# Performance work log

Measured on AMD Instinct MI355X. Metric: run time of the kernel, lower is better.

The kernel has to match this reference:

```python
import jax, jax.numpy as jnp
import numpy as np

N_EMBD = 1024
N_HEAD = 16
HEAD_DIM = N_EMBD // N_HEAD


def setup_inputs() -> dict:
    key = jax.random.key(0)
    kx, kq, kk, kv, ko = jax.random.split(key, 5)
    B, S = 2, 2048
    return {
        "x": jax.random.normal(kx, (B, S, N_EMBD), dtype=jnp.float32),
        "W_q": jax.random.normal(kq, (N_EMBD, N_EMBD), dtype=jnp.float32),
        "W_k": jax.random.normal(kk, (N_EMBD, N_EMBD), dtype=jnp.float32),
        "W_v": jax.random.normal(kv, (N_EMBD, N_EMBD), dtype=jnp.float32),
        "W_o": jax.random.normal(ko, (N_EMBD, N_EMBD), dtype=jnp.float32),
    }


def reference(x, W_q, W_k, W_v, W_o):
    B, S, E = x.shape
    H, D = N_HEAD, HEAD_DIM
    scale = 1.0 / np.sqrt(D).astype(np.float32)
    # QKV projections, split into heads: (B, H, S, D)
    q = (x @ W_q).reshape(B, S, H, D).transpose(0, 2, 1, 3)
    k = (x @ W_k).reshape(B, S, H, D).transpose(0, 2, 1, 3)
    v = (x @ W_v).reshape(B, S, H, D).transpose(0, 2, 1, 3)
    # scaled scores with causal mask
    scores = jnp.einsum("bhqd,bhkd->bhqk", q, k) * scale
    causal = jnp.tril(jnp.ones((S, S), dtype=bool))
    scores = jnp.where(causal, scores, -jnp.inf)
    attn = jax.nn.softmax(scores, axis=-1)
    out = jnp.einsum("bhqk,bhkd->bhqd", attn, v)
    out = out.transpose(0, 2, 1, 3).reshape(B, S, E)
    return out @ W_o
```

## Files before the change

kernel.cpp:

```cpp
#include <hip/hip_runtime.h>
#include <stdint.h>

#define E 1024
#define S 2048
#define NH 16
#define HD 64

typedef _Float16 f16;
typedef _Float16 f16x4 __attribute__((ext_vector_type(4)));
typedef _Float16 f16x8 __attribute__((ext_vector_type(8)));
typedef __fp16 hv4 __attribute__((ext_vector_type(4)));
typedef float f32x4 __attribute__((ext_vector_type(4)));

__device__ __forceinline__ void async16(const void* g, void* l) {
  __builtin_amdgcn_global_load_lds(
      (const __attribute__((address_space(1))) unsigned int*)g,
      (__attribute__((address_space(3))) unsigned int*)l, 16, 0, 0);
}

__global__ __launch_bounds__(256) void cvt_all(
    const float* __restrict__ x, const float* __restrict__ Wq,
    const float* __restrict__ Wk, const float* __restrict__ Wv,
    const float* __restrict__ Wo, f16* __restrict__ xh, f16* __restrict__ xl,
    f16* __restrict__ Wh, f16* __restrict__ Wl) {
  const int z = blockIdx.z;
  const int tid = threadIdx.x;
  if (z == 4) {
    int base = ((blockIdx.y * 32 + blockIdx.x) * 256 + tid) * 16;
#pragma unroll
    for (int u = 0; u < 4; u++) {
      int i = base + u * 4;
      float4 a = *(const float4*)(x + i);
      f16 h0 = (f16)a.x, h1 = (f16)a.y, h2 = (f16)a.z, h3 = (f16)a.w;
      f16x4 hv = {h0, h1, h2, h3};
      f16x4 lv = {(f16)(a.x - (float)h0), (f16)(a.y - (float)h1),
                  (f16)(a.z - (float)h2), (f16)(a.w - (float)h3)};
      *(f16x4*)(xh + i) = hv;
      *(f16x4*)(xl + i) = lv;
    }
    return;
  }
  __shared__ float tile[32][33];
  const float* W = z == 0 ? Wq : z == 1 ? Wk : z == 2 ? Wv : Wo;
  const int tx = tid & 31, ty = tid >> 5;
  const int x0 = blockIdx.x * 32, y0 = blockIdx.y * 32;
#pragma unroll
  for (int i = 0; i < 4; i++)
    tile[ty + i * 8][tx] = W[(size_t)(y0 + ty + i * 8) * E + x0 + tx];
  __syncthreads();
  f16* outh = Wh + (size_t)z * E * E;
  f16* outl = Wl + (size_t)z * E * E;
#pragma unroll
  for (int i = 0; i < 4; i++) {
    float v = tile[tx][ty + i * 8];
    size_t o = (size_t)(x0 + ty + i * 8) * E + (y0 + tx);
    f16 hi = (f16)v;
    outh[o] = hi;
    if (z < 2) outl[o] = (f16)(v - (float)hi);
  }
}


template <bool SPLIT2>
__device__ __forceinline__ void gemm_mainloop(
    const f16* __restrict__ Ah, const f16* __restrict__ Al,
    const f16* __restrict__ Bh, const f16* __restrict__ Bl, int m0, int n0,
    int K, f16* Ahs, f16* Als, f16* Bhs, f16* Bls, f32x4 acc[4][4]) {
  const int tid = threadIdx.x, lane = tid & 63, wid = tid >> 6;
  const int quad = lane >> 4, c16 = lane & 15;
  const int rA = tid >> 2;
  const int cA = (tid & 3) ^ ((rA >> 1) & 3);
  const size_t gA0 = (size_t)(m0 + rA) * K + cA * 8;
  const size_t gA1 = (size_t)(m0 + 64 + rA) * K + cA * 8;
  const size_t gB0 = (size_t)(n0 + rA) * K + cA * 8;
  const size_t gB1 = (size_t)(n0 + 64 + rA) * K + cA * 8;
  const int l0 = tid * 8, l1 = (256 + tid) * 8;
  int a_off[4], b_off[4];
#pragma unroll
  for (int i = 0; i < 4; i++) {
    int ra = (wid >> 1) * 64 + i * 16 + c16;
    a_off[i] = ra * 32 + ((quad ^ ((ra >> 1) & 3)) << 3);
    int rb = (wid & 1) * 64 + i * 16 + c16;
    b_off[i] = rb * 32 + ((quad ^ ((rb >> 1) & 3)) << 3);
  }
  for (int k0 = 0; k0 < K; k0 += 32) {
    __syncthreads();
    async16(Ah + gA0 + k0, Ahs + l0);
    async16(Ah + gA1 + k0, Ahs + l1);
    async16(Bh + gB0 + k0, Bhs + l0);
    async16(Bh + gB1 + k0, Bhs + l1);
    if constexpr (SPLIT2) {
      async16(Al + gA0 + k0, Als + l0);
      async16(Al + gA1 + k0, Als + l1);
      async16(Bl + gB0 + k0, Bls + l0);
      async16(Bl + gB1 + k0, Bls + l1);
    }
    __syncthreads();
    f16x8 ah[4], bh[4];
#pragma unroll
    for (int i = 0; i < 4; i++) {
      ah[i] = *(const f16x8*)(Ahs + a_off[i]);
      bh[i] = *(const f16x8*)(Bhs + b_off[i]);
    }
    if constexpr (SPLIT2) {
      f16x8 al[4], bl[4];
#pragma unroll
      for (int i = 0; i < 4; i++) {
        al[i] = *(const f16x8*)(Als + a_off[i]);
        bl[i] = *(const f16x8*)(Bls + b_off[i]);
      }
#pragma unroll
      for (int i = 0; i < 4; i++)
#pragma unroll
        for (int j = 0; j < 4; j++) {
          acc[i][j] = __builtin_amdgcn_mfma_f32_16x16x32_f16(ah[i], bh[j], acc[i][j], 0, 0, 0);
          acc[i][j] = __builtin_amdgcn_mfma_f32_16x16x32_f16(ah[i], bl[j], acc[i][j], 0, 0, 0);
          acc[i][j] = __builtin_amdgcn_mfma_f32_16x16x32_f16(al[i], bh[j], acc[i][j], 0, 0, 0);
        }
    } else {
#pragma unroll
      for (int i = 0; i < 4; i++)
#pragma unroll
        for (int j = 0; j < 4; j++)
          acc[i][j] = __builtin_amdgcn_mfma_f32_16x16x32_f16(ah[i], bh[j], acc[i][j], 0, 0, 0);
    }
  }
}

__global__ __launch_bounds__(256) void qkv_gemm(
    const f16* __restrict__ xh, const f16* __restrict__ xl,
    const f16* __restrict__ Wh, const f16* __restrict__ Wl,
    f16* __restrict__ Qh, f16* __restrict__ Ql, f16* __restrict__ Kh,
    f16* __restrict__ Kl, f16* __restrict__ Vt) {
  __shared__ __align__(16) char smem_raw[36864];
  f16* Ahs = (f16*)smem_raw;
  f16* Als = Ahs + 4096;
  f16* Bhs = Ahs + 8192;
  f16* Bls = Ahs + 12288;
  const int z = blockIdx.z;
  const int m0 = blockIdx.y * 128, n0 = blockIdx.x * 128;
  const f16* Bth = Wh + (size_t)z * E * E;
  const f16* Btl = Wl + (size_t)z * E * E;
  f32x4 acc[4][4];
  const f32x4 zero4 = {0.f, 0.f, 0.f, 0.f};
#pragma unroll
  for (int i = 0; i < 4; i++)
#pragma unroll
    for (int j = 0; j < 4; j++) acc[i][j] = zero4;
  if (z < 2)
    gemm_mainloop<true>(xh, xl, Bth, Btl, m0, n0, E, Ahs, Als, Bhs, Bls, acc);
  else
    gemm_mainloop<false>(xh, nullptr, Bth, nullptr, m0, n0, E, Ahs, Als, Bhs, Bls, acc);
  const int tid = threadIdx.x, lane = tid & 63, wid = tid >> 6;
  const int quad = lane >> 4, c16 = lane & 15;
  if (z == 2) {
    __syncthreads();
    f16* vbuf = (f16*)smem_raw + (size_t)wid * 4608;
#pragma unroll
    for (int i = 0; i < 4; i++)
#pragma unroll
      for (int j = 0; j < 4; j++)
#pragma unroll
        for (int r = 0; r < 4; r++) {
          int sl = i * 16 + quad * 4 + r;
          int dl = j * 16 + c16;
          vbuf[dl * 72 + sl] = (f16)acc[i][j][r];
        }
#pragma unroll
    for (int i2 = 0; i2 < 8; i2++) {
      int dl = i2 * 8 + (lane >> 3);
      int ck = lane & 7;
      f16x8 v8 = *(const f16x8*)(vbuf + dl * 72 + ck * 8);
      int dg = n0 + (wid & 1) * 64 + dl;
      int sg = m0 + (wid >> 1) * 64 + ck * 8;
      int b = sg >> 11, s = sg & (S - 1);
      int h = dg >> 6, d = dg & 63;
      *(f16x8*)(Vt + (((size_t)(b * NH + h) * HD + d) << 11) + s) = v8;
    }
  } else {
    const float sc = 0.42466090014400953f;
#pragma unroll
    for (int i = 0; i < 4; i++)
#pragma unroll
      for (int j = 0; j < 4; j++)
#pragma unroll
        for (int r = 0; r < 4; r++) {
          int row = m0 + (wid >> 1) * 64 + i * 16 + quad * 4 + r;
          int col = n0 + (wid & 1) * 64 + j * 16 + c16;
          int b = row >> 11, s = row & (S - 1);
          int h = col >> 6, d = col & 63;
          float v = acc[i][j][r] * sc;
          size_t idx = (((size_t)(b * NH + h) * S + s) << 6) + d;
          f16 hi = (f16)v;
          f16 lo = (f16)(v - (float)hi);
          if (z == 0) { Qh[idx] = hi; Ql[idx] = lo; }
          else        { Kh[idx] = hi; Kl[idx] = lo; }
        }
  }
}

__global__ __launch_bounds__(256, 3) void flash(
    const f16* __restrict__ Qh, const f16* __restrict__ Ql,
    const f16* __restrict__ Kh, const f16* __restrict__ Kl,
    const f16* __restrict__ Vt, f16* __restrict__ Ao) {
  __shared__ __align__(16) f16 Khs[2][4096], Kls[2][4096], Vs[2][4096];
  const int tid = threadIdx.x, lane = tid & 63, wid = tid >> 6;
  const int quad = lane >> 4, c16 = lane & 15;
  const int flat = blockIdx.y * 32 + blockIdx.x;
  const int xcd = flat & 7, slot = flat >> 3;
  const int bh = xcd * 4 + (slot >> 5);
  const int qtile = 31 - (slot & 31);
  const int q0 = qtile * 64;
  const size_t bhoff = (size_t)bh * S * HD;
  const int qbase = wid * 16;
  f16x8 qf_h[2], qf_l[2];
#pragma unroll
  for (int ks = 0; ks < 2; ks++) {
    int q = q0 + qbase + c16;
    size_t off = bhoff + (size_t)q * HD + ks * 32 + quad * 8;
    qf_h[ks] = *(const f16x8*)(Qh + off);
    qf_l[ks] = *(const f16x8*)(Ql + off);
  }
  const int niter = qtile + 1;
  const int s0 = tid, s1 = 256 + tid;
  const int r0 = s0 >> 3, cc0 = ((s0 & 7) ^ (r0 & 7)) * 8;
  const int r1 = s1 >> 3, cc1 = ((s1 & 7) ^ (r1 & 7)) * 8;
  auto stage = [&](int it, int b) {
    const size_t kb = bhoff + (size_t)(it * 64) * HD;
    async16(Kh + kb + r0 * HD + cc0, &Khs[b][s0 * 8]);
    async16(Kh + kb + r1 * HD + cc1, &Khs[b][s1 * 8]);
    async16(Kl + kb + r0 * HD + cc0, &Kls[b][s0 * 8]);
    async16(Kl + kb + r1 * HD + cc1, &Kls[b][s1 * 8]);
    const size_t vb = bhoff + (size_t)(it * 64);
    async16(Vt + vb + (size_t)r0 * S + cc0, &Vs[b][s0 * 8]);
    async16(Vt + vb + (size_t)r1 * S + cc1, &Vs[b][s1 * 8]);
  };
  stage(0, 0);
  float mrow = -3.0e38f, lsum = 0.f;
  f32x4 oacc[4];
  const f32x4 zero4 = {0.f, 0.f, 0.f, 0.f};
#pragma unroll
  for (int dt = 0; dt < 4; dt++) oacc[dt] = zero4;
  const int qrow = q0 + qbase + c16;
  for (int it = 0; it < niter; ++it) {
    const int cur = it & 1;
    __syncthreads();
    if (it + 1 < niter) stage(it + 1, cur ^ 1);
    const int k0 = it * 64;
    f32x4 st[4];
#pragma unroll
    for (int kt = 0; kt < 4; kt++) st[kt] = zero4;
#pragma unroll
    for (int kt = 0; kt < 4; kt++) {
      int rowk = (kt * 16 + c16) * 64;
      int sx = c16 & 7;
      f16x8 kh0 = *(const f16x8*)&Khs[cur][rowk + ((quad ^ sx) << 3)];
      f16x8 kh1 = *(const f16x8*)&Khs[cur][rowk + (((4 + quad) ^ sx) << 3)];
      f16x8 kl0 = *(const f16x8*)&Kls[cur][rowk + ((quad ^ sx) << 3)];
      f16x8 kl1 = *(const f16x8*)&Kls[cur][rowk + (((4 + quad) ^ sx) << 3)];
      st[kt] = __builtin_amdgcn_mfma_f32_16x16x32_f16(kh0, qf_h[0], st[kt], 0, 0, 0);
      st[kt] = __builtin_amdgcn_mfma_f32_16x16x32_f16(kh1, qf_h[1], st[kt], 0, 0, 0);
      st[kt] = __builtin_amdgcn_mfma_f32_16x16x32_f16(kh0, qf_l[0], st[kt], 0, 0, 0);
      st[kt] = __builtin_amdgcn_mfma_f32_16x16x32_f16(kh1, qf_l[1], st[kt], 0, 0, 0);
      st[kt] = __builtin_amdgcn_mfma_f32_16x16x32_f16(kl0, qf_h[0], st[kt], 0, 0, 0);
      st[kt] = __builtin_amdgcn_mfma_f32_16x16x32_f16(kl1, qf_h[1], st[kt], 0, 0, 0);
    }
    if (it == niter - 1) {
#pragma unroll
      for (int kt = 0; kt < 4; kt++) {
        int kb = k0 + kt * 16 + quad * 4;
#pragma unroll
        for (int r = 0; r < 4; r++)
          if (kb + r > qrow) st[kt][r] = -3.0e38f;
      }
    }
    float mx = -3.0e38f;
#pragma unroll
    for (int kt = 0; kt < 4; kt++) {
      float a = fmaxf(fmaxf(st[kt][0], st[kt][1]), fmaxf(st[kt][2], st[kt][3]));
      mx = fmaxf(mx, a);
    }
    mx = fmaxf(mx, __shfl_xor(mx, 16, 64));
    mx = fmaxf(mx, __shfl_xor(mx, 32, 64));
    float mn = fmaxf(mrow, mx);
    float alpha = __builtin_amdgcn_exp2f(mrow - mn);
    mrow = mn;
    float ls = lsum * alpha;
    hv4 pb[4];
#pragma unroll
    for (int kt = 0; kt < 4; kt++) {
      float p0 = __builtin_amdgcn_exp2f(st[kt][0] - mn);
      float p1 = __builtin_amdgcn_exp2f(st[kt][1] - mn);
      float p2 = __builtin_amdgcn_exp2f(st[kt][2] - mn);
      float p3 = __builtin_amdgcn_exp2f(st[kt][3] - mn);
      ls += (p0 + p1) + (p2 + p3);
      hv4 pv = {(__fp16)p0, (__fp16)p1, (__fp16)p2, (__fp16)p3};
      pb[kt] = pv;
    }
    lsum = ls;
#pragma unroll
    for (int dt = 0; dt < 4; dt++) {
      oacc[dt][0] *= alpha;
      oacc[dt][1] *= alpha;
      oacc[dt][2] *= alpha;
      oacc[dt][3] *= alpha;
    }
#pragma unroll
    for (int kt = 0; kt < 4; kt++) {
#pragma unroll
      for (int dt = 0; dt < 4; dt++) {
        int rowd = dt * 16 + c16;
        int cidx = (kt * 2 + (quad >> 1)) ^ (rowd & 7);
        hv4 vf = *(const hv4*)&Vs[cur][rowd * 64 + (cidx << 3) + (quad & 1) * 4];
        oacc[dt] = __builtin_amdgcn_mfma_f32_16x16x16f16(vf, pb[kt], oacc[dt], 0, 0, 0);
      }
    }
  }
  const int bb = bh >> 4, hh = bh & 15;
  float l = lsum;
  l += __shfl_xor(l, 16, 64);
  l += __shfl_xor(l, 32, 64);
  float iv = 1.0f / l;
  const int q = q0 + qbase + c16;
#pragma unroll
  for (int dt = 0; dt < 4; dt++) {
    f16x4 ov = {(f16)(oacc[dt][0] * iv), (f16)(oacc[dt][1] * iv),
                (f16)(oacc[dt][2] * iv), (f16)(oacc[dt][3] * iv)};
    *(f16x4*)(Ao + ((size_t)(bb * S + q)) * E + hh * 64 + dt * 16 + quad * 4) = ov;
  }
}

__global__ __launch_bounds__(256) void out_gemm(const f16* __restrict__ Ao,
                                                const f16* __restrict__ Wo,
                                                float* __restrict__ Cout) {
  __shared__ __align__(16) f16 Ahs[2048], Bhs[4096];
  const int tid = threadIdx.x, lane = tid & 63, wid = tid >> 6;
  const int quad = lane >> 4, c16 = lane & 15;
  const int m0 = blockIdx.y * 64, n0 = blockIdx.x * 128;
  f32x4 acc[4][2];
  const f32x4 zero4 = {0.f, 0.f, 0.f, 0.f};
#pragma unroll
  for (int i = 0; i < 4; i++)
#pragma unroll
    for (int j = 0; j < 2; j++) acc[i][j] = zero4;
  const int rA = tid >> 2;
  const int cA = (tid & 3) ^ ((rA >> 1) & 3);
  const size_t gA0 = (size_t)(m0 + rA) * E + cA * 8;
  const size_t gB0 = (size_t)(n0 + rA) * E + cA * 8;
  const size_t gB1 = (size_t)(n0 + 64 + rA) * E + cA * 8;
  const int l0 = tid * 8, l1 = (256 + tid) * 8;
  int a_off[4], b_off[2];
#pragma unroll
  for (int i = 0; i < 4; i++) {
    int ra = i * 16 + c16;
    a_off[i] = ra * 32 + ((quad ^ ((ra >> 1) & 3)) << 3);
  }
#pragma unroll
  for (int j = 0; j < 2; j++) {
    int rb = wid * 32 + j * 16 + c16;
    b_off[j] = rb * 32 + ((quad ^ ((rb >> 1) & 3)) << 3);
  }
  for (int k0 = 0; k0 < E; k0 += 32) {
    __syncthreads();
    async16(Ao + gA0 + k0, Ahs + l0);
    async16(Wo + gB0 + k0, Bhs + l0);
    async16(Wo + gB1 + k0, Bhs + l1);
    __syncthreads();
    f16x8 ah[4], bh[2];
#pragma unroll
    for (int i = 0; i < 4; i++) ah[i] = *(const f16x8*)(Ahs + a_off[i]);
#pragma unroll
    for (int j = 0; j < 2; j++) bh[j] = *(const f16x8*)(Bhs + b_off[j]);
#pragma unroll
    for (int i = 0; i < 4; i++)
#pragma unroll
      for (int j = 0; j < 2; j++)
        acc[i][j] = __builtin_amdgcn_mfma_f32_16x16x32_f16(ah[i], bh[j], acc[i][j], 0, 0, 0);
  }
#pragma unroll
  for (int i = 0; i < 4; i++)
#pragma unroll
    for (int j = 0; j < 2; j++)
#pragma unroll
      for (int r = 0; r < 4; r++) {
        int row = m0 + i * 16 + quad * 4 + r;
        int col = n0 + wid * 32 + j * 16 + c16;
        Cout[(size_t)row * E + col] = acc[i][j][r];
      }
}

extern "C" void kernel_launch(void* const* d_in, const int* in_sizes, int n_in,
                              void* d_out, int out_size, void* d_ws,
                              size_t ws_size, hipStream_t stream) {
  const float* x = (const float*)d_in[0];
  const float* Wq = (const float*)d_in[1];
  const float* Wk = (const float*)d_in[2];
  const float* Wv = (const float*)d_in[3];
  const float* Wo = (const float*)d_in[4];
  char* ws = (char*)d_ws;
  const size_t MB = (size_t)1 << 20;
  f16* xh = (f16*)(ws + 0 * MB);
  f16* xl = (f16*)(ws + 8 * MB);
  f16* Wh = (f16*)(ws + 16 * MB);
  f16* Wl = (f16*)(ws + 24 * MB);
  f16* Qh = (f16*)(ws + 28 * MB);
  f16* Ql = (f16*)(ws + 36 * MB);
  f16* Kh = (f16*)(ws + 44 * MB);
  f16* Kl = (f16*)(ws + 52 * MB);
  f16* Vt = (f16*)(ws + 60 * MB);
  f16* Ao = (f16*)(ws + 68 * MB);
  cvt_all<<<dim3(32, 32, 5), 256, 0, stream>>>(x, Wq, Wk, Wv, Wo, xh, xl, Wh, Wl);
  qkv_gemm<<<dim3(8, 32, 3), 256, 0, stream>>>(xh, xl, Wh, Wl, Qh, Ql, Kh, Kl, Vt);
  flash<<<dim3(32, 32), 256, 0, stream>>>(Qh, Ql, Kh, Kl, Vt, Ao);
  out_gemm<<<dim3(8, 64), 256, 0, stream>>>(Ao, Wh + (size_t)3 * E * E, (float*)d_out);
}
```

Baseline: 241.4 us.

## Double-buffer LDS tiles in QKV and output GEMMs and reorder block grid

New measurement: 236.4 us. -2.1%, faster.

```diff
diff --git a/kernel.cpp b/kernel.cpp
--- a/kernel.cpp
+++ b/kernel.cpp
@@ -83,31 +83,37 @@
     int rb = (wid & 1) * 64 + i * 16 + c16;
     b_off[i] = rb * 32 + ((quad ^ ((rb >> 1) & 3)) << 3);
   }
-  for (int k0 = 0; k0 < K; k0 += 32) {
+  auto stage = [&](int k0, int b) {
+    const int o = b << 12;
+    async16(Ah + gA0 + k0, Ahs + o + l0);
+    async16(Ah + gA1 + k0, Ahs + o + l1);
+    async16(Bh + gB0 + k0, Bhs + o + l0);
+    async16(Bh + gB1 + k0, Bhs + o + l1);
+    if constexpr (SPLIT2) {
+      async16(Al + gA0 + k0, Als + o + l0);
+      async16(Al + gA1 + k0, Als + o + l1);
+      async16(Bl + gB0 + k0, Bls + o + l0);
+      async16(Bl + gB1 + k0, Bls + o + l1);
+    }
+  };
+  stage(0, 0);
+  int cur = 0;
+  for (int k0 = 0; k0 < K; k0 += 32, cur ^= 1) {
     __syncthreads();
-    async16(Ah + gA0 + k0, Ahs + l0);
-    async16(Ah + gA1 + k0, Ahs + l1);
-    async16(Bh + gB0 + k0, Bhs + l0);
-    async16(Bh + gB1 + k0, Bhs + l1);
-    if constexpr (SPLIT2) {
-      async16(Al + gA0 + k0, Als + l0);
-      async16(Al + gA1 + k0, Als + l1);
-      async16(Bl + gB0 + k0, Bls + l0);
-      async16(Bl + gB1 + k0, Bls + l1);
-    }
-    __syncthreads();
+    if (k0 + 32 < K) stage(k0 + 32, cur ^ 1);
+    const int o = cur << 12;
     f16x8 ah[4], bh[4];
 #pragma unroll
     for (int i = 0; i < 4; i++) {
-      ah[i] = *(const f16x8*)(Ahs + a_off[i]);
-      bh[i] = *(const f16x8*)(Bhs + b_off[i]);
+      ah[i] = *(const f16x8*)(Ahs + o + a_off[i]);
+      bh[i] = *(const f16x8*)(Bhs + o + b_off[i]);
     }
     if constexpr (SPLIT2) {
       f16x8 al[4], bl[4];
 #pragma unroll
       for (int i = 0; i < 4; i++) {
-        al[i] = *(const f16x8*)(Als + a_off[i]);
-        bl[i] = *(const f16x8*)(Bls + b_off[i]);
+        al[i] = *(const f16x8*)(Als + o + a_off[i]);
+        bl[i] = *(const f16x8*)(Bls + o + b_off[i]);
       }
 #pragma unroll
       for (int i = 0; i < 4; i++)
@@ -132,13 +138,10 @@
     const f16* __restrict__ Wh, const f16* __restrict__ Wl,
     f16* __restrict__ Qh, f16* __restrict__ Ql, f16* __restrict__ Kh,
     f16* __restrict__ Kl, f16* __restrict__ Vt) {
-  __shared__ __align__(16) char smem_raw[36864];
-  f16* Ahs = (f16*)smem_raw;
-  f16* Als = Ahs + 4096;
-  f16* Bhs = Ahs + 8192;
-  f16* Bls = Ahs + 12288;
-  const int z = blockIdx.z;
-  const int m0 = blockIdx.y * 128, n0 = blockIdx.x * 128;
+  __shared__ __align__(16) f16 Ahs[2][4096], Als[2][4096], Bhs[2][4096],
+      Bls[2][4096];
+  const int z = blockIdx.y >> 3;
+  const int m0 = blockIdx.x * 128, n0 = (blockIdx.y & 7) * 128;
   const f16* Bth = Wh + (size_t)z * E * E;
   const f16* Btl = Wl + (size_t)z * E * E;
   f32x4 acc[4][4];
@@ -148,14 +151,16 @@
 #pragma unroll
     for (int j = 0; j < 4; j++) acc[i][j] = zero4;
   if (z < 2)
-    gemm_mainloop<true>(xh, xl, Bth, Btl, m0, n0, E, Ahs, Als, Bhs, Bls, acc);
+    gemm_mainloop<true>(xh, xl, Bth, Btl, m0, n0, E, &Ahs[0][0], &Als[0][0],
+                        &Bhs[0][0], &Bls[0][0], acc);
   else
-    gemm_mainloop<false>(xh, nullptr, Bth, nullptr, m0, n0, E, Ahs, Als, Bhs, Bls, acc);
+    gemm_mainloop<false>(xh, nullptr, Bth, nullptr, m0, n0, E, &Ahs[0][0],
+                         nullptr, &Bhs[0][0], nullptr, acc);
   const int tid = threadIdx.x, lane = tid & 63, wid = tid >> 6;
   const int quad = lane >> 4, c16 = lane & 15;
   if (z == 2) {
     __syncthreads();
-    f16* vbuf = (f16*)smem_raw + (size_t)wid * 4608;
+    f16* vbuf = &Ahs[0][0] + (size_t)wid * 4608;
 #pragma unroll
     for (int i = 0; i < 4; i++)
 #pragma unroll
@@ -333,10 +338,10 @@
 __global__ __launch_bounds__(256) void out_gemm(const f16* __restrict__ Ao,
                                                 const f16* __restrict__ Wo,
                                                 float* __restrict__ Cout) {
-  __shared__ __align__(16) f16 Ahs[2048], Bhs[4096];
+  __shared__ __align__(16) f16 Ahs[2][2048], Bhs[2][4096];
   const int tid = threadIdx.x, lane = tid & 63, wid = tid >> 6;
   const int quad = lane >> 4, c16 = lane & 15;
-  const int m0 = blockIdx.y * 64, n0 = blockIdx.x * 128;
+  const int m0 = blockIdx.x * 64, n0 = blockIdx.y * 128;
   f32x4 acc[4][2];
   const f32x4 zero4 = {0.f, 0.f, 0.f, 0.f};
 #pragma unroll
@@ -360,17 +365,21 @@
     int rb = wid * 32 + j * 16 + c16;
     b_off[j] = rb * 32 + ((quad ^ ((rb >> 1) & 3)) << 3);
   }
-  for (int k0 = 0; k0 < E; k0 += 32) {
+  auto stage = [&](int k0, int b) {
+    async16(Ao + gA0 + k0, &Ahs[b][0] + l0);
+    async16(Wo + gB0 + k0, &Bhs[b][0] + l0);
+    async16(Wo + gB1 + k0, &Bhs[b][0] + l1);
+  };
+  stage(0, 0);
+  int cur = 0;
+  for (int k0 = 0; k0 < E; k0 += 32, cur ^= 1) {
     __syncthreads();
-    async16(Ao + gA0 + k0, Ahs + l0);
-    async16(Wo + gB0 + k0, Bhs + l0);
-    async16(Wo + gB1 + k0, Bhs + l1);
-    __syncthreads();
+    if (k0 + 32 < E) stage(k0 + 32, cur ^ 1);
     f16x8 ah[4], bh[2];
 #pragma unroll
-    for (int i = 0; i < 4; i++) ah[i] = *(const f16x8*)(Ahs + a_off[i]);
-#pragma unroll
-    for (int j = 0; j < 2; j++) bh[j] = *(const f16x8*)(Bhs + b_off[j]);
+    for (int i = 0; i < 4; i++) ah[i] = *(const f16x8*)(&Ahs[cur][0] + a_off[i]);
+#pragma unroll
+    for (int j = 0; j < 2; j++) bh[j] = *(const f16x8*)(&Bhs[cur][0] + b_off[j]);
 #pragma unroll
     for (int i = 0; i < 4; i++)
 #pragma unroll
@@ -410,7 +419,7 @@
   f16* Vt = (f16*)(ws + 60 * MB);
   f16* Ao = (f16*)(ws + 68 * MB);
   cvt_all<<<dim3(32, 32, 5), 256, 0, stream>>>(x, Wq, Wk, Wv, Wo, xh, xl, Wh, Wl);
-  qkv_gemm<<<dim3(8, 32, 3), 256, 0, stream>>>(xh, xl, Wh, Wl, Qh, Ql, Kh, Kl, Vt);
+  qkv_gemm<<<dim3(32, 24), 256, 0, stream>>>(xh, xl, Wh, Wl, Qh, Ql, Kh, Kl, Vt);
   flash<<<dim3(32, 32), 256, 0, stream>>>(Qh, Ql, Kh, Kl, Vt, Ao);
-  out_gemm<<<dim3(8, 64), 256, 0, stream>>>(Ao, Wh + (size_t)3 * E * E, (float*)d_out);
-}
+  out_gemm<<<dim3(64, 8), 256, 0, stream>>>(Ao, Wh + (size_t)3 * E * E, (float*)d_out);
+}
```
